# Kernel optimization log

Hardware: AMD Instinct MI355X
Metric: run time of the kernel (lower is better)

Reference implementation:

```python
import jax, jax.numpy as jnp
import numpy as np

RATIO = 0.25
LN_EPS = 1e-5
D_IN = 512
D_OUT = 512


def setup_inputs() -> dict:
    key = jax.random.key(0)
    ks = jax.random.split(key, 8)
    B, N = 8, 16384
    features = jax.random.normal(ks[0], (B, N, D_IN), dtype=jnp.float32)
    coords = jax.random.uniform(ks[1], (B, N, 2), dtype=jnp.float32)
    times = jax.random.uniform(ks[2], (B, N), dtype=jnp.float32)
    polarities = jax.random.uniform(ks[3], (B, N), dtype=jnp.float32)
    # learned params: nn.Linear(D_IN, D_OUT) + nn.LayerNorm(D_OUT)
    W = jax.random.normal(ks[4], (D_OUT, D_IN), dtype=jnp.float32) / np.sqrt(D_IN)
    b = jnp.zeros((D_OUT,), dtype=jnp.float32)
    gamma = jnp.ones((D_OUT,), dtype=jnp.float32)
    beta = jnp.zeros((D_OUT,), dtype=jnp.float32)
    return {"features": features, "coords": coords, "times": times,
            "polarities": polarities, "W": W, "b": b, "gamma": gamma, "beta": beta}


def farthest_point_sample(coords, times, num_samples):
    # coords [B,N,2], times [B,N] -> indices [B,num_samples]
    B, N, _ = coords.shape
    points = jnp.concatenate([coords, times[..., None]], axis=-1)  # [B,N,3]
    first = jnp.zeros((B,), dtype=jnp.int32)  # deterministic seed point (torch uses randint)
    dist0 = jnp.full((B, N), jnp.inf, dtype=points.dtype)
    barange = jnp.arange(B)

    def step(carry, _):
        dist_min, last = carry
        last_pt = points[barange, last]                         # [B,3]
        d = jnp.sqrt(jnp.sum((points - last_pt[:, None, :]) ** 2, axis=-1) + 1e-8)
        dist_min = jnp.minimum(dist_min, d)                     # [B,N]
        nxt = jnp.argmax(dist_min, axis=-1).astype(jnp.int32)   # [B]
        return (dist_min, nxt), nxt

    (_, _), rest = jax.lax.scan(step, (dist0, first), None, length=num_samples - 1)
    # rest: [num_samples-1, B] -> [B, num_samples]
    return jnp.concatenate([first[:, None], rest.T], axis=1)


def layer_norm(x, gamma, beta):
    mu = jnp.mean(x, axis=-1, keepdims=True)
    var = jnp.mean((x - mu) ** 2, axis=-1, keepdims=True)
    return (x - mu) * jax.lax.rsqrt(var + LN_EPS) * gamma + beta


def reference(features, coords, times, polarities, W, b, gamma, beta):
    B, N, _ = features.shape
    M = max(int(N * RATIO), 1)
    idx = farthest_point_sample(coords, times, M)               # [B,M]
    feats_out = jnp.take_along_axis(features, idx[..., None], axis=1)   # [B,M,D_in]
    coords_out = jnp.take_along_axis(coords, idx[..., None], axis=1)    # [B,M,2]
    times_out = jnp.take_along_axis(times, idx, axis=1)                 # [B,M]
    pol_out = jnp.take_along_axis(polarities, idx, axis=1)              # [B,M]
    proj = jnp.einsum('bmd,od->bmo', feats_out, W) + b                  # [B,M,D_out]
    feats_out = layer_norm(proj, gamma, beta)
    return feats_out, coords_out, times_out, pol_out
```

## Files before the change

kernel.cpp:

```cpp
#include <hip/hip_runtime.h>
#include <math.h>

#define B_ 8
#define N_ 16384
#define M_ 4096
#define D_ 512
#define TPB 1024
#define PPT 16

#define FEAT_SZ (B_ * M_ * D_)
#define COFF FEAT_SZ
#define TOFF (FEAT_SZ + 2 * B_ * M_)
#define POFF (TOFF + B_ * M_)

#define R16(F) F(0) F(1) F(2) F(3) F(4) F(5) F(6) F(7) \
               F(8) F(9) F(10) F(11) F(12) F(13) F(14) F(15)
#define R16D(F) F(15) F(14) F(13) F(12) F(11) F(10) F(9) F(8) \
                F(7) F(6) F(5) F(4) F(3) F(2) F(1) F(0)

template <int CTRL>
__device__ __forceinline__ float dpp_max_step(float x) {
    const int y = __builtin_amdgcn_update_dpp(0, __float_as_int(x),
                                              CTRL, 0xf, 0xf, true);
    return fmaxf(x, __int_as_float(y));
}

__global__ __launch_bounds__(TPB)
__attribute__((amdgpu_waves_per_eu(4, 4)))
void fps_kernel(
    const float* __restrict__ coords, const float* __restrict__ times,
    int* __restrict__ idx_out)
{
    const int b = blockIdx.x;
    const int t = threadIdx.x;
    const float* cb = coords + (size_t)b * N_ * 2;
    const float* tb = times + (size_t)b * N_;

    __shared__ float2 cxy[N_];
    __shared__ __align__(16) float red_s[16];
    __shared__ unsigned long long nxt[2];

#define DECLV(i) float pt##i, m##i;
    R16(DECLV)
#undef DECLV

#define LOADV(i) { const int gi = (i) * TPB + t;                              \
        const float2 c2 = *(const float2*)(cb + 2 * (size_t)gi);              \
        cxy[gi] = c2; pt##i = tb[gi]; m##i = INFINITY; }
    R16(LOADV)
#undef LOADV

#define PINV(i) asm("" : "+v"(pt##i));
    R16(PINV)
#undef PINV

    if (t == 0) {
        idx_out[b * M_] = 0;
        nxt[0] = ~0ull; nxt[1] = ~0ull;
    }
    float lx = cb[0], ly = cb[1], lt = tb[0];
    __syncthreads();

    const int wave = t >> 6;
    const int lane = t & 63;

    for (int k = 1; k < M_; ++k) {
        const int par = k & 1;
        float bm = -INFINITY;

#define UPDV(i) {                                                             \
        const float2 c2 = cxy[(i) * TPB + t];                                 \
        const float dx = c2.x - lx;                                           \
        const float dy = c2.y - ly;                                           \
        const float dz = pt##i - lt;                                          \
        const float d2 = __fmaf_rn(dz, dz, __fmaf_rn(dx, dx,                  \
                                                     __fmul_rn(dy, dy)));     \
        m##i = fminf(m##i, d2);                                               \
        bm = fmaxf(bm, m##i); }
        R16(UPDV)
#undef UPDV

        const float s_local = __fsqrt_rn(__fadd_rn(bm, 1e-8f));

        float v = s_local;
        v = dpp_max_step<0x111>(v);
        v = dpp_max_step<0x112>(v);
        v = dpp_max_step<0x114>(v);
        v = dpp_max_step<0x118>(v);
        v = dpp_max_step<0x142>(v);
        v = dpp_max_step<0x143>(v);
        if (lane == 63) red_s[wave] = v;
        __syncthreads();

        if (t == 0) nxt[par ^ 1] = ~0ull;

        const float4* rp = (const float4*)red_s;
        const float4 r0 = rp[0], r1 = rp[1], r2 = rp[2], r3 = rp[3];
        const float s_star = fmaxf(
            fmaxf(fmaxf(fmaxf(r0.x, r0.y), fmaxf(r0.z, r0.w)),
                  fmaxf(fmaxf(r1.x, r1.y), fmaxf(r1.z, r1.w))),
            fmaxf(fmaxf(fmaxf(r2.x, r2.y), fmaxf(r2.z, r2.w)),
                  fmaxf(fmaxf(r3.x, r3.y), fmaxf(r3.z, r3.w))));

        if (s_local == s_star) {
            int   fj = 0x7fffffff;
            float ft = 0.f;
#define SELV(i) if (m##i == bm) { fj = (i) * TPB + t; ft = pt##i; }
            R16D(SELV)
#undef SELV

            const unsigned bmu = __float_as_uint(bm);
            const float thresh = __uint_as_float(bmu >= 32u ? bmu - 32u : 0u);
            float cnt = 0.f;
#define CNTV(i) cnt += (m##i >= thresh) ? 1.0f : 0.0f;
            R16(CNTV)
#undef CNTV
            if (cnt > 1.5f) {
#define FIXV(i) if (m##i >= thresh) {                                         \
                const float si = __fsqrt_rn(__fadd_rn(m##i, 1e-8f));          \
                if (si == s_local) { fj = (i) * TPB + t; ft = pt##i; } }
                R16D(FIXV)
#undef FIXV
            }
            atomicMin(&nxt[par],
                      (((unsigned long long)(unsigned)fj) << 32) |
                      __float_as_uint(ft));
        }
        __syncthreads();

        const unsigned long long wk = nxt[par];
        const int gi = (int)(wk >> 32);
        lt = __uint_as_float((unsigned)wk);
        const float2 wv = cxy[gi];
        lx = wv.x; ly = wv.y;
        if (t == 0) idx_out[b * M_ + k] = gi;
    }
}

__global__ __launch_bounds__(256) void gather_kernel(
    const float* __restrict__ coords, const float* __restrict__ times,
    const float* __restrict__ pol, const int* __restrict__ idx,
    float* __restrict__ out)
{
    int i = blockIdx.x * 256 + threadIdx.x;
    if (i >= B_ * M_) return;
    int b = i >> 12;
    int g = b * N_ + idx[i];
    float2 c2 = *(const float2*)(coords + 2 * (size_t)g);
    *(float2*)(out + COFF + 2 * (size_t)i) = c2;
    out[TOFF + i] = times[g];
    out[POFF + i] = pol[g];
}

#define BM 32
#define BN 128
#define BK 32

__global__ __launch_bounds__(256) void proj_kernel(
    const float* __restrict__ features, const float* __restrict__ W,
    const float* __restrict__ bias, const int* __restrict__ idx,
    float* __restrict__ out)
{
    __shared__ float a_lds[BK][BM + 4];
    __shared__ float w_lds[BK][BN];
    __shared__ int   src[BM];

    const int t = threadIdx.x;
    const int rowBase = blockIdx.x * BM;
    const int oBase = blockIdx.y * BN;

    if (t < BM) {
        int row = rowBase + t;
        int b = row >> 12;
        src[t] = b * N_ + idx[row];
    }
    __syncthreads();

    const int rt = t >> 5;
    const int ot = t & 31;
    const int lr = t >> 3;
    const int lk = (t & 7) * 4;

    float c[4][4] = {};

    for (int kc = 0; kc < D_; kc += BK) {
        {
            float4 v = *(const float4*)(features + (size_t)src[lr] * D_ + kc + lk);
            a_lds[lk + 0][lr] = v.x; a_lds[lk + 1][lr] = v.y;
            a_lds[lk + 2][lr] = v.z; a_lds[lk + 3][lr] = v.w;
        }
#pragma unroll
        for (int p = 0; p < 4; ++p) {
            int o = p * 32 + lr;
            float4 v = *(const float4*)(W + (size_t)(oBase + o) * D_ + kc + lk);
            w_lds[lk + 0][o] = v.x; w_lds[lk + 1][o] = v.y;
            w_lds[lk + 2][o] = v.z; w_lds[lk + 3][o] = v.w;
        }
        __syncthreads();

#pragma unroll
        for (int k = 0; k < BK; ++k) {
            float4 af = *(const float4*)&a_lds[k][rt * 4];
            float4 wf = *(const float4*)&w_lds[k][ot * 4];
            float av[4] = { af.x, af.y, af.z, af.w };
            float wv[4] = { wf.x, wf.y, wf.z, wf.w };
#pragma unroll
            for (int ri = 0; ri < 4; ++ri)
#pragma unroll
                for (int oi = 0; oi < 4; ++oi)
                    c[ri][oi] = fmaf(av[ri], wv[oi], c[ri][oi]);
        }
        __syncthreads();
    }

    float4 bv = *(const float4*)(bias + oBase + ot * 4);
    float bvv[4] = { bv.x, bv.y, bv.z, bv.w };
#pragma unroll
    for (int ri = 0; ri < 4; ++ri) {
        int row = rowBase + rt * 4 + ri;
        float4 o4;
        o4.x = c[ri][0] + bvv[0];
        o4.y = c[ri][1] + bvv[1];
        o4.z = c[ri][2] + bvv[2];
        o4.w = c[ri][3] + bvv[3];
        *(float4*)(out + (size_t)row * D_ + oBase + ot * 4) = o4;
    }
}

__global__ __launch_bounds__(256) void ln_kernel(
    float* __restrict__ out, const float* __restrict__ gamma,
    const float* __restrict__ beta)
{
    const int w = threadIdx.x >> 6;
    const int lane = threadIdx.x & 63;
    const size_t row = (size_t)blockIdx.x * 4 + w;
    float* p = out + row * D_;

    float4 v0 = *(const float4*)(p + lane * 8);
    float4 v1 = *(const float4*)(p + lane * 8 + 4);
    float x[8] = { v0.x, v0.y, v0.z, v0.w, v1.x, v1.y, v1.z, v1.w };

    float sum = 0.f;
#pragma unroll
    for (int i = 0; i < 8; ++i) sum += x[i];
#pragma unroll
    for (int off = 1; off < 64; off <<= 1) sum += __shfl_xor(sum, off);
    const float mu = sum * (1.0f / 512.0f);

    float sq = 0.f;
#pragma unroll
    for (int i = 0; i < 8; ++i) { float d = x[i] - mu; sq = fmaf(d, d, sq); }
#pragma unroll
    for (int off = 1; off < 64; off <<= 1) sq += __shfl_xor(sq, off);
    const float inv = rsqrtf(sq * (1.0f / 512.0f) + 1e-5f);

    float4 g0 = *(const float4*)(gamma + lane * 8);
    float4 g1 = *(const float4*)(gamma + lane * 8 + 4);
    float4 b0 = *(const float4*)(beta + lane * 8);
    float4 b1 = *(const float4*)(beta + lane * 8 + 4);
    float g[8] = { g0.x, g0.y, g0.z, g0.w, g1.x, g1.y, g1.z, g1.w };
    float be[8] = { b0.x, b0.y, b0.z, b0.w, b1.x, b1.y, b1.z, b1.w };

    float y[8];
#pragma unroll
    for (int i = 0; i < 8; ++i) y[i] = fmaf((x[i] - mu) * inv, g[i], be[i]);

    float4 o0 = { y[0], y[1], y[2], y[3] };
    float4 o1 = { y[4], y[5], y[6], y[7] };
    *(float4*)(p + lane * 8) = o0;
    *(float4*)(p + lane * 8 + 4) = o1;
}

extern "C" void kernel_launch(void* const* d_in, const int* in_sizes, int n_in,
                              void* d_out, int out_size, void* d_ws, size_t ws_size,
                              hipStream_t stream)
{
    const float* features   = (const float*)d_in[0];
    const float* coords     = (const float*)d_in[1];
    const float* times      = (const float*)d_in[2];
    const float* polarities = (const float*)d_in[3];
    const float* W          = (const float*)d_in[4];
    const float* bias       = (const float*)d_in[5];
    const float* gamma      = (const float*)d_in[6];
    const float* beta       = (const float*)d_in[7];
    float* out = (float*)d_out;

    int* idx = (int*)d_ws;

    fps_kernel<<<B_, TPB, 0, stream>>>(coords, times, idx);

    gather_kernel<<<(B_ * M_ + 255) / 256, 256, 0, stream>>>(
        coords, times, polarities, idx, out);

    dim3 pgrid(B_ * M_ / BM, D_ / BN);
    proj_kernel<<<pgrid, 256, 0, stream>>>(features, W, bias, idx, out);

    ln_kernel<<<B_ * M_ / 4, 256, 0, stream>>>(out, gamma, beta);
}
```

Before: 6.214 ms.

## Morton-sort points and skip FPS distance updates via bounding-box lower bound

```diff
diff --git a/kernel.cpp b/kernel.cpp
--- a/kernel.cpp
+++ b/kernel.cpp
@@ -15,8 +15,6 @@
 
 #define R16(F) F(0) F(1) F(2) F(3) F(4) F(5) F(6) F(7) \
                F(8) F(9) F(10) F(11) F(12) F(13) F(14) F(15)
-#define R16D(F) F(15) F(14) F(13) F(12) F(11) F(10) F(9) F(8) \
-                F(7) F(6) F(5) F(4) F(3) F(2) F(1) F(0)
 
 template <int CTRL>
 __device__ __forceinline__ float dpp_max_step(float x) {
@@ -25,40 +23,125 @@
     return fmaxf(x, __int_as_float(y));
 }
 
+__device__ __forceinline__ unsigned spread4(unsigned v) {
+    return (v & 1u) | ((v & 2u) << 2) | ((v & 4u) << 4) | ((v & 8u) << 6);
+}
+__device__ __forceinline__ unsigned mcode(float x, float y, float tt) {
+    unsigned mx = min((unsigned)(int)(x * 16.0f), 15u);
+    unsigned my = min((unsigned)(int)(y * 16.0f), 15u);
+    unsigned mt = min((unsigned)(int)(tt * 16.0f), 15u);
+    return spread4(mx) | (spread4(my) << 1) | (spread4(mt) << 2);
+}
+
+__global__ __launch_bounds__(TPB) void msort_kernel(
+    const float* __restrict__ coords, const float* __restrict__ times,
+    float* __restrict__ sortx, float* __restrict__ sorty,
+    float* __restrict__ sortt, unsigned* __restrict__ sortid)
+{
+    const int b = blockIdx.x, t = threadIdx.x;
+    const float* cb = coords + (size_t)b * N_ * 2;
+    const float* tb = times + (size_t)b * N_;
+    const size_t bo = (size_t)b * N_;
+
+    __shared__ unsigned cnt[4096];
+    __shared__ unsigned wsum[TPB];
+
+    for (int i = t; i < 4096; i += TPB) cnt[i] = 0;
+    __syncthreads();
+
+    for (int j = 0; j < PPT; ++j) {
+        const int gi = j * TPB + t;
+        const float2 c2 = *(const float2*)(cb + 2 * (size_t)gi);
+        atomicAdd(&cnt[mcode(c2.x, c2.y, tb[gi])], 1u);
+    }
+    __syncthreads();
+
+    {
+        const unsigned c0 = cnt[4 * t], c1 = cnt[4 * t + 1],
+                       c2 = cnt[4 * t + 2], c3 = cnt[4 * t + 3];
+        wsum[t] = c0 + c1 + c2 + c3;
+        __syncthreads();
+        if (t == 0) {
+            unsigned run = 0;
+            for (int i = 0; i < TPB; ++i) { unsigned v = wsum[i]; wsum[i] = run; run += v; }
+        }
+        __syncthreads();
+        const unsigned base = wsum[t];
+        cnt[4 * t] = base;
+        cnt[4 * t + 1] = base + c0;
+        cnt[4 * t + 2] = base + c0 + c1;
+        cnt[4 * t + 3] = base + c0 + c1 + c2;
+    }
+    __syncthreads();
+
+    for (int j = 0; j < PPT; ++j) {
+        const int gi = j * TPB + t;
+        const float2 c2 = *(const float2*)(cb + 2 * (size_t)gi);
+        const float tt = tb[gi];
+        const unsigned pos = atomicAdd(&cnt[mcode(c2.x, c2.y, tt)], 1u);
+        sortx[bo + pos] = c2.x;
+        sorty[bo + pos] = c2.y;
+        sortt[bo + pos] = tt;
+        sortid[bo + pos] = (unsigned)gi;
+    }
+}
+
 __global__ __launch_bounds__(TPB)
 __attribute__((amdgpu_waves_per_eu(4, 4)))
 void fps_kernel(
     const float* __restrict__ coords, const float* __restrict__ times,
+    const float* __restrict__ sortx, const float* __restrict__ sorty,
+    const float* __restrict__ sortt, const unsigned* __restrict__ sortid,
     int* __restrict__ idx_out)
 {
     const int b = blockIdx.x;
     const int t = threadIdx.x;
     const float* cb = coords + (size_t)b * N_ * 2;
     const float* tb = times + (size_t)b * N_;
+    const size_t bo = (size_t)b * N_;
 
     __shared__ float2 cxy[N_];
     __shared__ __align__(16) float red_s[16];
-    __shared__ unsigned long long nxt[2];
+    __shared__ unsigned long long nxt_pos[2], nxt_t[2];
 
 #define DECLV(i) float pt##i, m##i;
     R16(DECLV)
 #undef DECLV
-
-#define LOADV(i) { const int gi = (i) * TPB + t;                              \
-        const float2 c2 = *(const float2*)(cb + 2 * (size_t)gi);              \
-        cxy[gi] = c2; pt##i = tb[gi]; m##i = INFINITY; }
+    unsigned id2_0, id2_1, id2_2, id2_3, id2_4, id2_5, id2_6, id2_7;
+
+    float bx0 = 1e30f, bx1 = -1e30f, by0 = 1e30f, by1 = -1e30f,
+          bt0 = 1e30f, bt1 = -1e30f;
+
+#define LOADV(i) { const int p = t * PPT + (i);                               \
+        const float x = sortx[bo + p], y = sorty[bo + p], tt = sortt[bo + p]; \
+        float2 v2; v2.x = x; v2.y = y;                                        \
+        cxy[(i) * TPB + t] = v2;                                              \
+        pt##i = tt; m##i = INFINITY;                                          \
+        bx0 = fminf(bx0, x); bx1 = fmaxf(bx1, x);                             \
+        by0 = fminf(by0, y); by1 = fmaxf(by1, y);                             \
+        bt0 = fminf(bt0, tt); bt1 = fmaxf(bt1, tt); }
     R16(LOADV)
 #undef LOADV
+
+#define LOADID(r) id2_##r = (sortid[bo + t * PPT + 2 * (r)] & 0xffffu) |      \
+                            (sortid[bo + t * PPT + 2 * (r) + 1] << 16);
+    LOADID(0) LOADID(1) LOADID(2) LOADID(3)
+    LOADID(4) LOADID(5) LOADID(6) LOADID(7)
+#undef LOADID
 
 #define PINV(i) asm("" : "+v"(pt##i));
     R16(PINV)
 #undef PINV
+    asm("" : "+v"(id2_0), "+v"(id2_1), "+v"(id2_2), "+v"(id2_3));
+    asm("" : "+v"(id2_4), "+v"(id2_5), "+v"(id2_6), "+v"(id2_7));
 
     if (t == 0) {
         idx_out[b * M_] = 0;
-        nxt[0] = ~0ull; nxt[1] = ~0ull;
+        nxt_pos[0] = nxt_pos[1] = ~0ull;
+        nxt_t[0] = nxt_t[1] = ~0ull;
     }
     float lx = cb[0], ly = cb[1], lt = tb[0];
+    float TM = INFINITY;
     __syncthreads();
 
     const int wave = t >> 6;
@@ -66,21 +149,32 @@
 
     for (int k = 1; k < M_; ++k) {
         const int par = k & 1;
-        float bm = -INFINITY;
-
-#define UPDV(i) {                                                             \
-        const float2 c2 = cxy[(i) * TPB + t];                                 \
-        const float dx = c2.x - lx;                                           \
-        const float dy = c2.y - ly;                                           \
-        const float dz = pt##i - lt;                                          \
-        const float d2 = __fmaf_rn(dz, dz, __fmaf_rn(dx, dx,                  \
+
+        const float ddx = fmaxf(fmaxf(bx0 - lx, lx - bx1), 0.0f);
+        const float ddy = fmaxf(fmaxf(by0 - ly, ly - by1), 0.0f);
+        const float ddt = fmaxf(fmaxf(bt0 - lt, lt - bt1), 0.0f);
+        const float lb2 = __fmaf_rn(ddt, ddt,
+                          __fmaf_rn(ddx, ddx, __fmul_rn(ddy, ddy)));
+
+        if (!(lb2 * 0.999996f >= TM)) {
+#define UPDV(i) { const float2 c2 = cxy[(i) * TPB + t];                       \
+            const float dx = c2.x - lx;                                       \
+            const float dy = c2.y - ly;                                       \
+            const float dz = pt##i - lt;                                      \
+            const float d2 = __fmaf_rn(dz, dz, __fmaf_rn(dx, dx,              \
                                                      __fmul_rn(dy, dy)));     \
-        m##i = fminf(m##i, d2);                                               \
-        bm = fmaxf(bm, m##i); }
-        R16(UPDV)
+            m##i = fminf(m##i, d2); }
+            R16(UPDV)
 #undef UPDV
-
-        const float s_local = __fsqrt_rn(__fadd_rn(bm, 1e-8f));
+            const float a0 = fmaxf(fmaxf(m0, m1), m2);
+            const float a1 = fmaxf(fmaxf(m3, m4), m5);
+            const float a2 = fmaxf(fmaxf(m6, m7), m8);
+            const float a3 = fmaxf(fmaxf(m9, m10), m11);
+            const float a4 = fmaxf(fmaxf(m12, m13), m14);
+            TM = fmaxf(fmaxf(fmaxf(a0, a1), a2), fmaxf(fmaxf(a3, a4), m15));
+        }
+
+        const float s_local = __fsqrt_rn(__fadd_rn(TM, 1e-8f));
 
         float v = s_local;
         v = dpp_max_step<0x111>(v);
@@ -92,7 +186,7 @@
         if (lane == 63) red_s[wave] = v;
         __syncthreads();
 
-        if (t == 0) nxt[par ^ 1] = ~0ull;
+        if (t == 0) { nxt_pos[par ^ 1] = ~0ull; nxt_t[par ^ 1] = ~0ull; }
 
         const float4* rp = (const float4*)red_s;
         const float4 r0 = rp[0], r1 = rp[1], r2 = rp[2], r3 = rp[3];
@@ -103,35 +197,59 @@
                   fmaxf(fmaxf(r3.x, r3.y), fmaxf(r3.z, r3.w))));
 
         if (s_local == s_star) {
-            int   fj = 0x7fffffff;
-            float ft = 0.f;
-#define SELV(i) if (m##i == bm) { fj = (i) * TPB + t; ft = pt##i; }
-            R16D(SELV)
-#undef SELV
+            const float bm = TM;
+            unsigned bid = 0xffffffffu; unsigned bpos = 0; float bt_ = 0.0f;
+
+#define SEL1(j, reg, sh) if (m##j == bm) {                                    \
+            const unsigned idj = ((reg) >> (sh)) & 0xffffu;                   \
+            if (idj < bid) { bid = idj; bpos = (unsigned)(t * PPT + (j));     \
+                             bt_ = pt##j; } }
+            SEL1(0, id2_0, 0)  SEL1(1, id2_0, 16)
+            SEL1(2, id2_1, 0)  SEL1(3, id2_1, 16)
+            SEL1(4, id2_2, 0)  SEL1(5, id2_2, 16)
+            SEL1(6, id2_3, 0)  SEL1(7, id2_3, 16)
+            SEL1(8, id2_4, 0)  SEL1(9, id2_4, 16)
+            SEL1(10, id2_5, 0) SEL1(11, id2_5, 16)
+            SEL1(12, id2_6, 0) SEL1(13, id2_6, 16)
+            SEL1(14, id2_7, 0) SEL1(15, id2_7, 16)
+#undef SEL1
 
             const unsigned bmu = __float_as_uint(bm);
             const float thresh = __uint_as_float(bmu >= 32u ? bmu - 32u : 0u);
-            float cnt = 0.f;
-#define CNTV(i) cnt += (m##i >= thresh) ? 1.0f : 0.0f;
+            float cntw = 0.0f;
+#define CNTV(i) cntw += (m##i >= thresh) ? 1.0f : 0.0f;
             R16(CNTV)
 #undef CNTV
-            if (cnt > 1.5f) {
-#define FIXV(i) if (m##i >= thresh) {                                         \
-                const float si = __fsqrt_rn(__fadd_rn(m##i, 1e-8f));          \
-                if (si == s_local) { fj = (i) * TPB + t; ft = pt##i; } }
-                R16D(FIXV)
-#undef FIXV
+            if (cntw > 1.5f) {
+                bid = 0xffffffffu; bpos = 0; bt_ = 0.0f;
+#define FIX1(j, reg, sh) if (m##j >= thresh) {                                \
+                const float sj = __fsqrt_rn(__fadd_rn(m##j, 1e-8f));          \
+                if (sj == s_local) {                                          \
+                    const unsigned idj = ((reg) >> (sh)) & 0xffffu;           \
+                    if (idj < bid) { bid = idj;                               \
+                        bpos = (unsigned)(t * PPT + (j)); bt_ = pt##j; } } }
+                FIX1(0, id2_0, 0)  FIX1(1, id2_0, 16)
+                FIX1(2, id2_1, 0)  FIX1(3, id2_1, 16)
+                FIX1(4, id2_2, 0)  FIX1(5, id2_2, 16)
+                FIX1(6, id2_3, 0)  FIX1(7, id2_3, 16)
+                FIX1(8, id2_4, 0)  FIX1(9, id2_4, 16)
+                FIX1(10, id2_5, 0) FIX1(11, id2_5, 16)
+                FIX1(12, id2_6, 0) FIX1(13, id2_6, 16)
+                FIX1(14, id2_7, 0) FIX1(15, id2_7, 16)
+#undef FIX1
             }
-            atomicMin(&nxt[par],
-                      (((unsigned long long)(unsigned)fj) << 32) |
-                      __float_as_uint(ft));
-        }
-        __syncthreads();
-
-        const unsigned long long wk = nxt[par];
-        const int gi = (int)(wk >> 32);
-        lt = __uint_as_float((unsigned)wk);
-        const float2 wv = cxy[gi];
+            const unsigned long long hi = ((unsigned long long)bid) << 32;
+            atomicMin(&nxt_pos[par], hi | bpos);
+            atomicMin(&nxt_t[par], hi | __float_as_uint(bt_));
+        }
+        __syncthreads();
+
+        const unsigned long long kp = nxt_pos[par];
+        const unsigned long long kt = nxt_t[par];
+        const int gi = (int)(kp >> 32);
+        const unsigned pos = (unsigned)kp;
+        lt = __uint_as_float((unsigned)kt);
+        const float2 wv = cxy[(pos & 15u) * TPB + (pos >> 4)];
         lx = wv.x; ly = wv.y;
         if (t == 0) idx_out[b * M_ + k] = gi;
     }
@@ -286,8 +404,15 @@
     float* out = (float*)d_out;
 
     int* idx = (int*)d_ws;
-
-    fps_kernel<<<B_, TPB, 0, stream>>>(coords, times, idx);
+    float* sortx = (float*)((char*)d_ws + (size_t)B_ * M_ * 4);
+    float* sorty = sortx + (size_t)B_ * N_;
+    float* sortt = sorty + (size_t)B_ * N_;
+    unsigned* sortid = (unsigned*)(sortt + (size_t)B_ * N_);
+
+    msort_kernel<<<B_, TPB, 0, stream>>>(coords, times, sortx, sorty, sortt, sortid);
+
+    fps_kernel<<<B_, TPB, 0, stream>>>(coords, times, sortx, sorty, sortt,
+                                       sortid, idx);
 
     gather_kernel<<<(B_ * M_ + 255) / 256, 256, 0, stream>>>(
         coords, times, polarities, idx, out);
```

New measurement: 6.516 ms. +4.9%, slower.
